# Kernel tuning notes

Hardware: AMD Instinct MI355X
Metric: run time of the kernel (lower is better)

The kernel has to match this reference:

```python
import jax, jax.numpy as jnp
import numpy as np

H = W = 256
WS = 8          # window size
SHIFT = 4       # shift size
HEADS = 8
DIM = 128
HD = DIM // HEADS
EPS = 1e-5


def _rel_index():
    # Swin-style relative position index, static constant (N=WS*WS)
    coords = np.stack(np.meshgrid(np.arange(WS), np.arange(WS), indexing='ij')).reshape(2, -1)
    rel = coords[:, :, None] - coords[:, None, :]        # (2, N, N)
    rel = rel + (WS - 1)
    return rel[0] * (2 * WS - 1) + rel[1]                # (N, N) in [0, (2WS-1)^2)

_REL_IDX = _rel_index()


def _ln(x, w, b):
    m = jnp.mean(x, axis=-1, keepdims=True)
    v = jnp.var(x, axis=-1, keepdims=True)
    return (x - m) * jax.lax.rsqrt(v + EPS) * w + b


def setup_inputs() -> dict:
    key = jax.random.key(0)
    ks = jax.random.split(key, 8)
    s = 0.02
    return {
        'x': jax.random.normal(ks[0], (2, H * W, DIM), jnp.float32),
        'norm1_w': jnp.ones((DIM,), jnp.float32),
        'norm1_b': jnp.zeros((DIM,), jnp.float32),
        'qkv_w': jax.random.normal(ks[1], (3 * DIM, DIM), jnp.float32) * s,
        'qkv_b': jnp.zeros((3 * DIM,), jnp.float32),
        'rel_bias_table': jax.random.normal(ks[2], ((2 * WS - 1) ** 2, HEADS), jnp.float32) * s,
        'proj_w': jax.random.normal(ks[3], (DIM, DIM), jnp.float32) * s,
        'proj_b': jnp.zeros((DIM,), jnp.float32),
        'norm2_w': jnp.ones((DIM,), jnp.float32),
        'norm2_b': jnp.zeros((DIM,), jnp.float32),
        'fc1_w': jax.random.normal(ks[4], (4 * DIM, DIM), jnp.float32) * s,
        'fc1_b': jnp.zeros((4 * DIM,), jnp.float32),
        'fc2_w': jax.random.normal(ks[5], (DIM, 4 * DIM), jnp.float32) * s,
        'fc2_b': jnp.zeros((DIM,), jnp.float32),
    }


def reference(x, norm1_w, norm1_b, qkv_w, qkv_b, rel_bias_table, proj_w, proj_b,
              norm2_w, norm2_b, fc1_w, fc1_b, fc2_w, fc2_b):
    B, L, C = x.shape
    N = WS * WS
    shortcut = x

    # norm1 -> spatial -> shift (roll only; original applies no attention mask)
    xs = _ln(x, norm1_w, norm1_b).reshape(B, H, W, C)
    xs = jnp.roll(xs, shift=(-SHIFT, -SHIFT), axis=(1, 2))

    # window partition: (B*nH*nW, N, C)
    win = xs.reshape(B, H // WS, WS, W // WS, WS, C)
    win = win.transpose(0, 1, 3, 2, 4, 5).reshape(-1, N, C)

    # window attention
    qkv = (win @ qkv_w.T + qkv_b).reshape(-1, N, 3, HEADS, HD)
    qkv = qkv.transpose(2, 0, 3, 1, 4)                   # (3, nWin, heads, N, hd)
    q, k, v = qkv[0], qkv[1], qkv[2]
    scale = HD ** -0.5
    attn = jnp.einsum('whnd,whmd->whnm', q * scale, k)   # (nWin, heads, N, N)
    bias = rel_bias_table[_REL_IDX]                      # (N, N, heads)
    attn = attn + bias.transpose(2, 0, 1)[None]
    attn = jax.nn.softmax(attn, axis=-1)
    out = jnp.einsum('whnm,whmd->whnd', attn, v)         # (nWin, heads, N, hd)
    out = out.transpose(0, 2, 1, 3).reshape(-1, N, C)
    out = out @ proj_w.T + proj_b

    # window reverse + un-shift
    out = out.reshape(B, H // WS, W // WS, WS, WS, C)
    out = out.transpose(0, 1, 3, 2, 4, 5).reshape(B, H, W, C)
    out = jnp.roll(out, shift=(SHIFT, SHIFT), axis=(1, 2)).reshape(B, L, C)

    x = shortcut + out

    # MLP (fc1 -> exact GELU -> fc2) with residual
    h = _ln(x, norm2_w, norm2_b)
    h = jax.nn.gelu(h @ fc1_w.T + fc1_b, approximate=False)
    h = h @ fc2_w.T + fc2_b
    return x + h
```

## Files before the change

### kernel.cpp

```cpp
#include <hip/hip_runtime.h>
#include <hip/hip_bf16.h>
#include <cmath>

#define LNEPS 1e-5f

typedef __attribute__((ext_vector_type(8))) short short8v;
typedef __attribute__((ext_vector_type(4))) float f32x4;

__device__ __forceinline__ unsigned short f2bf(float f){
  unsigned u = __float_as_uint(f);
  u += 0x7fffu + ((u >> 16) & 1u);
  return (unsigned short)(u >> 16);
}
__device__ __forceinline__ float gelu_f(float x){
  return 0.5f * x * (1.f + erff(x * 0.70710678118654752f));
}

__device__ __forceinline__ f32x4 mfma32(short8v a, short8v b, f32x4 c){
#ifdef __HIP_DEVICE_COMPILE__
  return __builtin_amdgcn_mfma_f32_16x16x32_bf16(a, b, c, 0, 0, 0);
#else
  return c;
#endif
}

__device__ __forceinline__ void stage128(const unsigned short* g, int ldg, short* lds){
#ifdef __HIP_DEVICE_COMPILE__
  const int t = threadIdx.x;
  const int wv = t >> 6;
  #pragma unroll
  for (int it = 0; it < 8; ++it) {
    const int flat = it * 256 + t;
    const int r = flat >> 4, c = flat & 15;
    const unsigned short* src = g + (size_t)r * ldg + ((c ^ (r & 7)) << 3);
    short* dst = lds + (size_t)(it * 256 + wv * 64) * 8;
    __builtin_amdgcn_global_load_lds(
        (const __attribute__((address_space(1))) void*)src,
        (__attribute__((address_space(3))) void*)dst, 16, 0, 0);
  }
#else
  (void)g; (void)ldg; (void)lds;
#endif
}
__device__ __forceinline__ void stage128_512(const unsigned short* g, int ldg, short* lds){
#ifdef __HIP_DEVICE_COMPILE__
  const int t = threadIdx.x;
  const int wv = t >> 6;
  #pragma unroll
  for (int it = 0; it < 4; ++it) {
    const int flat = it * 512 + t;
    const int r = flat >> 4, c = flat & 15;
    const unsigned short* src = g + (size_t)r * ldg + ((c ^ (r & 7)) << 3);
    short* dst = lds + (size_t)(it * 512 + wv * 64) * 8;
    __builtin_amdgcn_global_load_lds(
        (const __attribute__((address_space(1))) void*)src,
        (__attribute__((address_space(3))) void*)dst, 16, 0, 0);
  }
#else
  (void)g; (void)ldg; (void)lds;
#endif
}
__device__ __forceinline__ void stage64(const unsigned short* g, short* lds){
#ifdef __HIP_DEVICE_COMPILE__
  const int t = threadIdx.x;
  const int wv = t >> 6;
  #pragma unroll
  for (int it = 0; it < 4; ++it) {
    const int flat = it * 256 + t;
    const int r = flat >> 4, c = flat & 15;
    const unsigned short* src = g + (size_t)r * 128 + ((c ^ (r & 7)) << 3);
    short* dst = lds + (size_t)(it * 256 + wv * 64) * 8;
    __builtin_amdgcn_global_load_lds(
        (const __attribute__((address_space(1))) void*)src,
        (__attribute__((address_space(3))) void*)dst, 16, 0, 0);
  }
#else
  (void)g; (void)lds;
#endif
}
__device__ __forceinline__ short8v frag_ld(const short* lds, int row, int chunk){
  return *(const short8v*)((const char*)lds + row * 256 + ((chunk ^ (row & 7)) << 4));
}

__global__ __launch_bounds__(256) void k0_cvt(
    const float* __restrict__ qkvw, const float* __restrict__ pw,
    const float* __restrict__ w1, const float* __restrict__ w2,
    unsigned short* __restrict__ dst)
{
  const int i = (blockIdx.x * 256 + threadIdx.x) * 4;
  const float* src; int off;
  if (i < 49152)       { src = qkvw; off = i; }
  else if (i < 65536)  { src = pw;   off = i - 49152; }
  else if (i < 131072) { src = w1;   off = i - 65536; }
  else                 { src = w2;   off = i - 131072; }
  const float4 v = *(const float4*)(src + off);
  ushort4 o = { f2bf(v.x), f2bf(v.y), f2bf(v.z), f2bf(v.w) };
  *(ushort4*)(dst + i) = o;
}

__global__ __launch_bounds__(512, 2) void k23_qkv_attn(
    const float* __restrict__ x,
    const float* __restrict__ gw, const float* __restrict__ gb,
    const unsigned short* __restrict__ Wb,
    const float* __restrict__ bias,
    const float* __restrict__ table,
    unsigned short* __restrict__ attn)
{
  __shared__ __align__(16) short At[128 * 128];
  __shared__ __align__(16) short Bt[128 * 128];
  __shared__ __align__(16) short QKl[128 * 256];
  __shared__ float Tb[1800];
  const int t = threadIdx.x;
  const int row0 = blockIdx.x * 128;
  stage128_512(Wb, 128, At);
  for (int i = t; i < 1800; i += 512) Tb[i] = table[i];
  #pragma unroll
  for (int it = 0; it < 4; ++it) {
    const int flat = it * 512 + t;
    const int r = flat >> 4, c = flat & 15;
    const int row = row0 + r;
    const int wid = row >> 6, n = row & 63;
    const int b = wid >> 10, rem = wid & 1023;
    const int wh = rem >> 5, wwi = rem & 31;
    const int i2 = n >> 3, j2 = n & 7;
    const int sh = (wh * 8 + i2 + 4) & 255;
    const int sw = (wwi * 8 + j2 + 4) & 255;
    const float* src = x + (((size_t)b << 16) + sh * 256 + sw) * 128 + c * 8;
    const float4 a0 = *(const float4*)src;
    const float4 a1 = *(const float4*)(src + 4);
    float s  = a0.x + a0.y + a0.z + a0.w + a1.x + a1.y + a1.z + a1.w;
    float ss = a0.x*a0.x + a0.y*a0.y + a0.z*a0.z + a0.w*a0.w
             + a1.x*a1.x + a1.y*a1.y + a1.z*a1.z + a1.w*a1.w;
    s += __shfl_xor(s, 1); ss += __shfl_xor(ss, 1);
    s += __shfl_xor(s, 2); ss += __shfl_xor(ss, 2);
    s += __shfl_xor(s, 4); ss += __shfl_xor(ss, 4);
    s += __shfl_xor(s, 8); ss += __shfl_xor(ss, 8);
    const float mean = s * 0.0078125f;
    const float rstd = rsqrtf(ss * 0.0078125f - mean * mean + LNEPS);
    const float4 g0 = *(const float4*)(gw + c * 8), g1 = *(const float4*)(gw + c * 8 + 4);
    const float4 c0 = *(const float4*)(gb + c * 8), c1 = *(const float4*)(gb + c * 8 + 4);
    uint4 pk;
    pk.x = (unsigned)f2bf((a0.x - mean) * rstd * g0.x + c0.x)
         | ((unsigned)f2bf((a0.y - mean) * rstd * g0.y + c0.y) << 16);
    pk.y = (unsigned)f2bf((a0.z - mean) * rstd * g0.z + c0.z)
         | ((unsigned)f2bf((a0.w - mean) * rstd * g0.w + c0.w) << 16);
    pk.z = (unsigned)f2bf((a1.x - mean) * rstd * g1.x + c1.x)
         | ((unsigned)f2bf((a1.y - mean) * rstd * g1.y + c1.y) << 16);
    pk.w = (unsigned)f2bf((a1.z - mean) * rstd * g1.z + c1.z)
         | ((unsigned)f2bf((a1.w - mean) * rstd * g1.w + c1.w) << 16);
    *(uint4*)((char*)Bt + r * 256 + ((c ^ (r & 7)) << 4)) = pk;
  }
  __syncthreads();

  const int l = t & 63, w = t >> 6, w0 = w & 1, w1 = w >> 1;
  const int g = l >> 4, rl = l & 15;
  const f32x4 z = {0.f, 0.f, 0.f, 0.f};

  for (int nt = 0; nt < 3; ++nt) {
    f32x4 acc[4][2];
    #pragma unroll
    for (int i = 0; i < 4; ++i) { acc[i][0] = z; acc[i][1] = z; }
    #pragma unroll
    for (int kk = 0; kk < 4; ++kk) {
      short8v a[4], b[2];
      #pragma unroll
      for (int i = 0; i < 4; ++i) a[i] = frag_ld(At, w0 * 64 + i * 16 + rl, kk * 4 + g);
      #pragma unroll
      for (int j = 0; j < 2; ++j) b[j] = frag_ld(Bt, w1 * 32 + j * 16 + rl, kk * 4 + g);
      #pragma unroll
      for (int i = 0; i < 4; ++i)
        #pragma unroll
        for (int j = 0; j < 2; ++j)
          acc[i][j] = mfma32(a[i], b[j], acc[i][j]);
    }
    if (nt < 2) {
      #pragma unroll
      for (int i = 0; i < 4; ++i) {
        const int c = w0 * 64 + i * 16 + 4 * g;
        const float4 bv = *(const float4*)(bias + nt * 128 + c);
        const int chunk = nt * 16 + (c >> 3), inner = (c & 7) * 2;
        #pragma unroll
        for (int j = 0; j < 2; ++j) {
          const int r = w1 * 32 + j * 16 + rl;
          ushort4 o = { f2bf(acc[i][j][0] + bv.x), f2bf(acc[i][j][1] + bv.y),
                        f2bf(acc[i][j][2] + bv.z), f2bf(acc[i][j][3] + bv.w) };
          *(ushort4*)((char*)QKl + r * 512 + ((chunk ^ (r & 7)) << 4) + inner) = o;
        }
      }
      __syncthreads();
      stage128_512(Wb + (size_t)(nt + 1) * 16384, 128, At);
      __syncthreads();
    } else {
      __syncthreads();
      #pragma unroll
      for (int i = 0; i < 4; ++i) {
        const int c = w0 * 64 + i * 16 + 4 * g;
        const int h2 = c >> 4, db = c & 15;
        const float4 bv = *(const float4*)(bias + 256 + c);
        const float ba[4] = {bv.x, bv.y, bv.z, bv.w};
        #pragma unroll
        for (int j = 0; j < 2; ++j) {
          const int r = w1 * 32 + j * 16 + rl;
          const int wl = r >> 6, m = r & 63;
          char* vb = (char*)Bt + (wl * 8 + h2) * 2048;
          #pragma unroll
          for (int e = 0; e < 4; ++e) {
            const int d = db + e;
            *(unsigned short*)(vb + d * 128 + (((m >> 3) ^ (d & 7)) << 4) + (m & 7) * 2)
                = f2bf(acc[i][j][e] + ba[e]);
          }
        }
      }
      __syncthreads();
    }
  }

  const int h = w;
  char* Pw = (char*)At + w * 4096;
  const short8v zz = {0,0,0,0,0,0,0,0};
  for (int wl = 0; wl < 2; ++wl) {
    const int win = blockIdx.x * 2 + wl;
    short8v qf[4], kf[4];
    if (g < 2) {
      #pragma unroll
      for (int rf = 0; rf < 4; ++rf) {
        const int r = wl * 64 + rf * 16 + rl;
        qf[rf] = *(const short8v*)((char*)QKl + r * 512 + (((2 * h + g) ^ (r & 7)) << 4));
      }
      #pragma unroll
      for (int mf = 0; mf < 4; ++mf) {
        const int r = wl * 64 + mf * 16 + rl;
        kf[mf] = *(const short8v*)((char*)QKl + r * 512 + (((16 + 2 * h + g) ^ (r & 7)) << 4));
      }
    } else {
      #pragma unroll
      for (int i = 0; i < 4; ++i) { qf[i] = zz; kf[i] = zz; }
    }
    f32x4 s[4][4];
    #pragma unroll
    for (int mf = 0; mf < 4; ++mf)
      #pragma unroll
      for (int rf = 0; rf < 4; ++rf)
        s[mf][rf] = mfma32(kf[mf], qf[rf], z);
    float sum[4];
    #pragma unroll
    for (int rf = 0; rf < 4; ++rf) {
      const int r = rf * 16 + rl, i1 = r >> 3, j1 = r & 7;
      float mx = -1e30f;
      #pragma unroll
      for (int mf = 0; mf < 4; ++mf)
        #pragma unroll
        for (int e = 0; e < 4; ++e) {
          const int m = mf * 16 + g * 4 + e;
          const int i2 = m >> 3, j2 = m & 7;
          const float v = s[mf][rf][e] * 0.25f + Tb[((i1 - i2 + 7) * 15 + (j1 - j2 + 7)) * 8 + h];
          s[mf][rf][e] = v;
          mx = fmaxf(mx, v);
        }
      mx = fmaxf(mx, __shfl_xor(mx, 16));
      mx = fmaxf(mx, __shfl_xor(mx, 32));
      float sm = 0.f;
      #pragma unroll
      for (int mf = 0; mf < 4; ++mf)
        #pragma unroll
        for (int e = 0; e < 4; ++e) {
          const float ev = __expf(s[mf][rf][e] - mx);
          s[mf][rf][e] = ev;
          sm += ev;
        }
      sm += __shfl_xor(sm, 16);
      sm += __shfl_xor(sm, 32);
      sum[rf] = sm;
    }
    const char* vbase = (char*)Bt + (wl * 8 + h) * 2048;
    f32x4 o[4];
    #pragma unroll
    for (int rf = 0; rf < 4; ++rf) o[rf] = z;
    #pragma unroll
    for (int hm = 0; hm < 2; ++hm) {
      #pragma unroll
      for (int rf = 0; rf < 4; ++rf) {
        const int r = rf * 16 + rl;
        #pragma unroll
        for (int mfl = 0; mfl < 2; ++mfl) {
          const int mf = hm * 2 + mfl;
          uint2 u;
          u.x = (unsigned)f2bf(s[mf][rf][0]) | ((unsigned)f2bf(s[mf][rf][1]) << 16);
          u.y = (unsigned)f2bf(s[mf][rf][2]) | ((unsigned)f2bf(s[mf][rf][3]) << 16);
          *(uint2*)(Pw + r * 64 + (((mfl * 2 + (g >> 1)) ^ ((r >> 1) & 3)) << 4) + (g & 1) * 8) = u;
        }
      }
      const short8v va = *(const short8v*)(vbase + rl * 128 + (((hm * 4 + g) ^ (rl & 7)) << 4));
      #pragma unroll
      for (int rf = 0; rf < 4; ++rf) {
        const int r = rf * 16 + rl;
        const short8v pb = *(const short8v*)(Pw + r * 64 + ((g ^ ((r >> 1) & 3)) << 4));
        o[rf] = mfma32(va, pb, o[rf]);
      }
    }
    #pragma unroll
    for (int rf = 0; rf < 4; ++rf) {
      const float inv = 1.f / sum[rf];
      const int r = rf * 16 + rl;
      ushort4 ov = { f2bf(o[rf][0] * inv), f2bf(o[rf][1] * inv),
                     f2bf(o[rf][2] * inv), f2bf(o[rf][3] * inv) };
      *(ushort4*)(attn + ((size_t)win * 64 + r) * 128 + h * 16 + g * 4) = ov;
    }
  }
}

__global__ __launch_bounds__(256, 2) void k45_proj_mlp(
    const unsigned short* __restrict__ A,
    const unsigned short* __restrict__ pwb,
    const float* __restrict__ pb,
    const float* __restrict__ xin,
    const float* __restrict__ gw, const float* __restrict__ gb,
    const unsigned short* __restrict__ w1b, const float* __restrict__ b1,
    const unsigned short* __restrict__ w2b, const float* __restrict__ b2,
    float* __restrict__ out)
{
  __shared__ __align__(16) short Xt[64 * 128];
  __shared__ __align__(16) short Ht[64 * 128];
  __shared__ __align__(16) short Wt[128 * 128];
  __shared__ float2 Gt[1024];
  __shared__ float2 Red[64 * 8];
  const int t = threadIdx.x;
  const int row0 = blockIdx.x * 64;
  stage128(pwb, 128, Wt);
  stage64(A + (size_t)row0 * 128, Ht);
  #pragma unroll
  for (int i = t; i < 1024; i += 256) {
    const float x0 = (float)i * 0.0078125f - 4.f;
    const float g0 = gelu_f(x0);
    Gt[i] = make_float2(g0, gelu_f(x0 + 0.0078125f) - g0);
  }
  const int l = t & 63, w = t >> 6, w0 = w & 1, w1 = w >> 1;
  const int g = l >> 4, rl = l & 15;
  size_t obase[2];
  float4 xv[4][2];
  #pragma unroll
  for (int j = 0; j < 2; ++j) {
    const int r = row0 + w1 * 32 + j * 16 + rl;
    const int wn = r >> 6, n = r & 63;
    const int b_ = wn >> 10, rem = wn & 1023;
    const int wh = rem >> 5, ww = rem & 31;
    const int si = n >> 3, sj = n & 7;
    const int hd = (wh * 8 + si + 4) & 255;
    const int wd = (ww * 8 + sj + 4) & 255;
    obase[j] = (((size_t)b_ << 16) + hd * 256 + wd) * 128;
    #pragma unroll
    for (int i = 0; i < 4; ++i)
      xv[i][j] = *(const float4*)(xin + obase[j] + w0 * 64 + i * 16 + 4 * g);
  }
  __syncthreads();
  const f32x4 z = {0.f, 0.f, 0.f, 0.f};
  f32x4 x2r[4][2];
  #pragma unroll
  for (int i = 0; i < 4; ++i) { x2r[i][0] = z; x2r[i][1] = z; }
  #pragma unroll
  for (int kk = 0; kk < 4; ++kk) {
    short8v a[4], b[2];
    #pragma unroll
    for (int i = 0; i < 4; ++i) a[i] = frag_ld(Wt, w0 * 64 + i * 16 + rl, kk * 4 + g);
    #pragma unroll
    for (int j = 0; j < 2; ++j) b[j] = frag_ld(Ht, w1 * 32 + j * 16 + rl, kk * 4 + g);
    #pragma unroll
    for (int i = 0; i < 4; ++i)
      #pragma unroll
      for (int j = 0; j < 2; ++j)
        x2r[i][j] = mfma32(a[i], b[j], x2r[i][j]);
  }
  #pragma unroll
  for (int i = 0; i < 4; ++i) {
    const float4 bv = *(const float4*)(pb + w0 * 64 + i * 16 + 4 * g);
    #pragma unroll
    for (int j = 0; j < 2; ++j) {
      x2r[i][j][0] += xv[i][j].x + bv.x;
      x2r[i][j][1] += xv[i][j].y + bv.y;
      x2r[i][j][2] += xv[i][j].z + bv.z;
      x2r[i][j][3] += xv[i][j].w + bv.w;
    }
  }
  #pragma unroll
  for (int j = 0; j < 2; ++j) {
    float s = 0.f, ss = 0.f;
    #pragma unroll
    for (int i = 0; i < 4; ++i)
      #pragma unroll
      for (int e = 0; e < 4; ++e) { const float v = x2r[i][j][e]; s += v; ss += v * v; }
    Red[(w1 * 32 + j * 16 + rl) * 8 + (w0 * 4 + g)] = make_float2(s, ss);
  }
  __syncthreads();
  float mean[2], rstd[2];
  #pragma unroll
  for (int j = 0; j < 2; ++j) {
    const float2* rp = &Red[(w1 * 32 + j * 16 + rl) * 8];
    float s = 0.f, ss = 0.f;
    #pragma unroll
    for (int k = 0; k < 8; ++k) { s += rp[k].x; ss += rp[k].y; }
    mean[j] = s * 0.0078125f;
    rstd[j] = rsqrtf(ss * 0.0078125f - mean[j] * mean[j] + LNEPS);
  }
  #pragma unroll
  for (int i = 0; i < 4; ++i) {
    const int c = w0 * 64 + i * 16 + 4 * g;
    const float4 g4 = *(const float4*)(gw + c);
    const float4 c4 = *(const float4*)(gb + c);
    #pragma unroll
    for (int j = 0; j < 2; ++j) {
      const int r = w1 * 32 + j * 16 + rl;
      ushort4 p;
      p.x = f2bf((x2r[i][j][0] - mean[j]) * rstd[j] * g4.x + c4.x);
      p.y = f2bf((x2r[i][j][1] - mean[j]) * rstd[j] * g4.y + c4.y);
      p.z = f2bf((x2r[i][j][2] - mean[j]) * rstd[j] * g4.z + c4.z);
      p.w = f2bf((x2r[i][j][3] - mean[j]) * rstd[j] * g4.w + c4.w);
      const int chunk = c >> 3, inner = (c & 7) * 2;
      *(ushort4*)((char*)Xt + r * 256 + ((chunk ^ (r & 7)) << 4) + inner) = p;
    }
  }
  f32x4 oacc[4][2];
  #pragma unroll
  for (int i = 0; i < 4; ++i) { oacc[i][0] = z; oacc[i][1] = z; }
  for (int sb = 0; sb < 4; ++sb) {
    __syncthreads();
    stage128(w1b + (size_t)sb * 128 * 128, 128, Wt);
    __syncthreads();
    f32x4 hacc[4][2];
    #pragma unroll
    for (int i = 0; i < 4; ++i) { hacc[i][0] = z; hacc[i][1] = z; }
    #pragma unroll
    for (int kk = 0; kk < 4; ++kk) {
      short8v a[4], b[2];
      #pragma unroll
      for (int i = 0; i < 4; ++i) a[i] = frag_ld(Wt, w0 * 64 + i * 16 + rl, kk * 4 + g);
      #pragma unroll
      for (int j = 0; j < 2; ++j) b[j] = frag_ld(Xt, w1 * 32 + j * 16 + rl, kk * 4 + g);
      #pragma unroll
      for (int i = 0; i < 4; ++i)
        #pragma unroll
        for (int j = 0; j < 2; ++j)
          hacc[i][j] = mfma32(a[i], b[j], hacc[i][j]);
    }
    __syncthreads();
    #pragma unroll
    for (int i = 0; i < 4; ++i) {
      const int cl = w0 * 64 + i * 16 + 4 * g;
      const float4 b1v = *(const float4*)(b1 + sb * 128 + cl);
      const float ba[4] = {b1v.x, b1v.y, b1v.z, b1v.w};
      #pragma unroll
      for (int j = 0; j < 2; ++j) {
        const int r = w1 * 32 + j * 16 + rl;
        unsigned short pe[4];
        #pragma unroll
        for (int e = 0; e < 4; ++e) {
          const float xh = hacc[i][j][e] + ba[e];
          float tq = fmaf(xh, 128.f, 512.f);
          tq = fminf(fmaxf(tq, 0.f), 1023.99f);
          const float fi = floorf(tq);
          const float2 ent = Gt[(int)fi];
          float gv = fmaf(tq - fi, ent.y, ent.x);
          gv = xh > 3.98f ? xh : gv;
          pe[e] = f2bf(gv);
        }
        ushort4 p = { pe[0], pe[1], pe[2], pe[3] };
        const int chunk = cl >> 3, inner = (cl & 7) * 2;
        *(ushort4*)((char*)Ht + r * 256 + ((chunk ^ (r & 7)) << 4) + inner) = p;
      }
    }
    stage128(w2b + (size_t)sb * 128, 512, Wt);
    __syncthreads();
    #pragma unroll
    for (int kk = 0; kk < 4; ++kk) {
      short8v a[4], b[2];
      #pragma unroll
      for (int i = 0; i < 4; ++i) a[i] = frag_ld(Wt, w0 * 64 + i * 16 + rl, kk * 4 + g);
      #pragma unroll
      for (int j = 0; j < 2; ++j) b[j] = frag_ld(Ht, w1 * 32 + j * 16 + rl, kk * 4 + g);
      #pragma unroll
      for (int i = 0; i < 4; ++i)
        #pragma unroll
        for (int j = 0; j < 2; ++j)
          oacc[i][j] = mfma32(a[i], b[j], oacc[i][j]);
    }
  }
  #pragma unroll
  for (int i = 0; i < 4; ++i) {
    const int c = w0 * 64 + i * 16 + 4 * g;
    const float4 bv = *(const float4*)(b2 + c);
    #pragma unroll
    for (int j = 0; j < 2; ++j) {
      float4 o = { x2r[i][j][0] + oacc[i][j][0] + bv.x,
                   x2r[i][j][1] + oacc[i][j][1] + bv.y,
                   x2r[i][j][2] + oacc[i][j][2] + bv.z,
                   x2r[i][j][3] + oacc[i][j][3] + bv.w };
      *(float4*)(out + obase[j] + c) = o;
    }
  }
}

extern "C" void kernel_launch(void* const* d_in, const int* in_sizes, int n_in,
                              void* d_out, int out_size, void* d_ws, size_t ws_size,
                              hipStream_t stream)
{
  const float* x    = (const float*)d_in[0];
  const float* n1w  = (const float*)d_in[1];
  const float* n1b  = (const float*)d_in[2];
  const float* qkvw = (const float*)d_in[3];
  const float* qkvB = (const float*)d_in[4];
  const float* relb = (const float*)d_in[5];
  const float* pw   = (const float*)d_in[6];
  const float* pb   = (const float*)d_in[7];
  const float* n2w  = (const float*)d_in[8];
  const float* n2b  = (const float*)d_in[9];
  const float* w1   = (const float*)d_in[10];
  const float* b1   = (const float*)d_in[11];
  const float* w2   = (const float*)d_in[12];
  const float* b2   = (const float*)d_in[13];
  float* out = (float*)d_out;

  unsigned short* winb = (unsigned short*)d_ws;
  unsigned short* wb   = winb + 16777216;
  unsigned short* qkvw_b = wb;
  unsigned short* pw_b   = wb + 49152;
  unsigned short* w1_b   = wb + 65536;
  unsigned short* w2_b   = wb + 131072;

  k0_cvt<<<192, 256, 0, stream>>>(qkvw, pw, w1, w2, wb);
  k23_qkv_attn<<<1024, 512, 0, stream>>>(x, n1w, n1b, qkvw_b, qkvB, relb, winb);
  k45_proj_mlp<<<2048, 256, 0, stream>>>(winb, pw_b, pb, x, n2w, n2b,
                                         w1_b, b1, w2_b, b2, out);
}
```

Before: 177.2 us.

## Fuse window attention with projection and MLP into one kernel

Merges the QKV+attention kernel and the proj+MLP kernel into a single 512-thread kernel, so attention outputs stay in LDS instead of round-tripping a 32MB bf16 buffer through global memory. The MLP stage is re-tiled so each wave owns 16 rows across all 128 output columns, which lets LayerNorm2 reduce with wave shuffles instead of an LDS reduction. The costs are a roughly 143KB LDS footprint that permits only one block per CU despite the launch bound of 2, a larger live register set, and a longer serial dependency chain per block.

```diff
diff --git a/kernel.cpp b/kernel.cpp
--- a/kernel.cpp
+++ b/kernel.cpp
@@ -24,24 +24,6 @@
 #endif
 }
 
-__device__ __forceinline__ void stage128(const unsigned short* g, int ldg, short* lds){
-#ifdef __HIP_DEVICE_COMPILE__
-  const int t = threadIdx.x;
-  const int wv = t >> 6;
-  #pragma unroll
-  for (int it = 0; it < 8; ++it) {
-    const int flat = it * 256 + t;
-    const int r = flat >> 4, c = flat & 15;
-    const unsigned short* src = g + (size_t)r * ldg + ((c ^ (r & 7)) << 3);
-    short* dst = lds + (size_t)(it * 256 + wv * 64) * 8;
-    __builtin_amdgcn_global_load_lds(
-        (const __attribute__((address_space(1))) void*)src,
-        (__attribute__((address_space(3))) void*)dst, 16, 0, 0);
-  }
-#else
-  (void)g; (void)ldg; (void)lds;
-#endif
-}
 __device__ __forceinline__ void stage128_512(const unsigned short* g, int ldg, short* lds){
 #ifdef __HIP_DEVICE_COMPILE__
   const int t = threadIdx.x;
@@ -58,24 +40,6 @@
   }
 #else
   (void)g; (void)ldg; (void)lds;
-#endif
-}
-__device__ __forceinline__ void stage64(const unsigned short* g, short* lds){
-#ifdef __HIP_DEVICE_COMPILE__
-  const int t = threadIdx.x;
-  const int wv = t >> 6;
-  #pragma unroll
-  for (int it = 0; it < 4; ++it) {
-    const int flat = it * 256 + t;
-    const int r = flat >> 4, c = flat & 15;
-    const unsigned short* src = g + (size_t)r * 128 + ((c ^ (r & 7)) << 3);
-    short* dst = lds + (size_t)(it * 256 + wv * 64) * 8;
-    __builtin_amdgcn_global_load_lds(
-        (const __attribute__((address_space(1))) void*)src,
-        (__attribute__((address_space(3))) void*)dst, 16, 0, 0);
-  }
-#else
-  (void)g; (void)lds;
 #endif
 }
 __device__ __forceinline__ short8v frag_ld(const short* lds, int row, int chunk){
@@ -98,22 +62,32 @@
   *(ushort4*)(dst + i) = o;
 }
 
-__global__ __launch_bounds__(512, 2) void k23_qkv_attn(
+__global__ __launch_bounds__(512, 2) void kfull(
     const float* __restrict__ x,
-    const float* __restrict__ gw, const float* __restrict__ gb,
-    const unsigned short* __restrict__ Wb,
-    const float* __restrict__ bias,
+    const float* __restrict__ g1w, const float* __restrict__ g1b,
+    const unsigned short* __restrict__ qkvWb, const float* __restrict__ qkvB,
     const float* __restrict__ table,
-    unsigned short* __restrict__ attn)
+    const unsigned short* __restrict__ pwb, const float* __restrict__ pb,
+    const float* __restrict__ g2w, const float* __restrict__ g2b,
+    const unsigned short* __restrict__ w1b, const float* __restrict__ b1,
+    const unsigned short* __restrict__ w2b, const float* __restrict__ b2,
+    float* __restrict__ out)
 {
-  __shared__ __align__(16) short At[128 * 128];
-  __shared__ __align__(16) short Bt[128 * 128];
-  __shared__ __align__(16) short QKl[128 * 256];
-  __shared__ float Tb[1800];
+  __shared__ __align__(16) char LP[146464];
+  short*  At  = (short*)LP;
+  short*  Bt  = (short*)(LP + 32768);
+  short*  QKl = (short*)(LP + 65536);
+  float*  Tb  = (float*)(LP + 131072);
+  float2* Gt  = (float2*)(LP + 138272);
   const int t = threadIdx.x;
   const int row0 = blockIdx.x * 128;
-  stage128_512(Wb, 128, At);
+  stage128_512(qkvWb, 128, At);
   for (int i = t; i < 1800; i += 512) Tb[i] = table[i];
+  for (int i = t; i < 1024; i += 512) {
+    const float x0 = (float)i * 0.0078125f - 4.f;
+    const float g0 = gelu_f(x0);
+    Gt[i] = make_float2(g0, gelu_f(x0 + 0.0078125f) - g0);
+  }
   #pragma unroll
   for (int it = 0; it < 4; ++it) {
     const int flat = it * 512 + t;
@@ -137,8 +111,8 @@
     s += __shfl_xor(s, 8); ss += __shfl_xor(ss, 8);
     const float mean = s * 0.0078125f;
     const float rstd = rsqrtf(ss * 0.0078125f - mean * mean + LNEPS);
-    const float4 g0 = *(const float4*)(gw + c * 8), g1 = *(const float4*)(gw + c * 8 + 4);
-    const float4 c0 = *(const float4*)(gb + c * 8), c1 = *(const float4*)(gb + c * 8 + 4);
+    const float4 g0 = *(const float4*)(g1w + c * 8), g1 = *(const float4*)(g1w + c * 8 + 4);
+    const float4 c0 = *(const float4*)(g1b + c * 8), c1 = *(const float4*)(g1b + c * 8 + 4);
     uint4 pk;
     pk.x = (unsigned)f2bf((a0.x - mean) * rstd * g0.x + c0.x)
          | ((unsigned)f2bf((a0.y - mean) * rstd * g0.y + c0.y) << 16);
@@ -152,7 +126,7 @@
   }
   __syncthreads();
 
-  const int l = t & 63, w = t >> 6, w0 = w & 1, w1 = w >> 1;
+  const int l = t & 63, w = t >> 6, w0 = w & 1, w1q = w >> 1;
   const int g = l >> 4, rl = l & 15;
   const f32x4 z = {0.f, 0.f, 0.f, 0.f};
 
@@ -166,7 +140,7 @@
       #pragma unroll
       for (int i = 0; i < 4; ++i) a[i] = frag_ld(At, w0 * 64 + i * 16 + rl, kk * 4 + g);
       #pragma unroll
-      for (int j = 0; j < 2; ++j) b[j] = frag_ld(Bt, w1 * 32 + j * 16 + rl, kk * 4 + g);
+      for (int j = 0; j < 2; ++j) b[j] = frag_ld(Bt, w1q * 32 + j * 16 + rl, kk * 4 + g);
       #pragma unroll
       for (int i = 0; i < 4; ++i)
         #pragma unroll
@@ -177,18 +151,18 @@
       #pragma unroll
       for (int i = 0; i < 4; ++i) {
         const int c = w0 * 64 + i * 16 + 4 * g;
-        const float4 bv = *(const float4*)(bias + nt * 128 + c);
+        const float4 bv = *(const float4*)(qkvB + nt * 128 + c);
         const int chunk = nt * 16 + (c >> 3), inner = (c & 7) * 2;
         #pragma unroll
         for (int j = 0; j < 2; ++j) {
-          const int r = w1 * 32 + j * 16 + rl;
+          const int r = w1q * 32 + j * 16 + rl;
           ushort4 o = { f2bf(acc[i][j][0] + bv.x), f2bf(acc[i][j][1] + bv.y),
                         f2bf(acc[i][j][2] + bv.z), f2bf(acc[i][j][3] + bv.w) };
           *(ushort4*)((char*)QKl + r * 512 + ((chunk ^ (r & 7)) << 4) + inner) = o;
         }
       }
       __syncthreads();
-      stage128_512(Wb + (size_t)(nt + 1) * 16384, 128, At);
+      stage128_512(qkvWb + (size_t)(nt + 1) * 16384, 128, At);
       __syncthreads();
     } else {
       __syncthreads();
@@ -196,11 +170,11 @@
       for (int i = 0; i < 4; ++i) {
         const int c = w0 * 64 + i * 16 + 4 * g;
         const int h2 = c >> 4, db = c & 15;
-        const float4 bv = *(const float4*)(bias + 256 + c);
+        const float4 bv = *(const float4*)(qkvB + 256 + c);
         const float ba[4] = {bv.x, bv.y, bv.z, bv.w};
         #pragma unroll
         for (int j = 0; j < 2; ++j) {
-          const int r = w1 * 32 + j * 16 + rl;
+          const int r = w1q * 32 + j * 16 + rl;
           const int wl = r >> 6, m = r & 63;
           char* vb = (char*)Bt + (wl * 8 + h2) * 2048;
           #pragma unroll
@@ -218,8 +192,8 @@
   const int h = w;
   char* Pw = (char*)At + w * 4096;
   const short8v zz = {0,0,0,0,0,0,0,0};
+  f32x4 o2[2][4];
   for (int wl = 0; wl < 2; ++wl) {
-    const int win = blockIdx.x * 2 + wl;
     short8v qf[4], kf[4];
     if (g < 2) {
       #pragma unroll
@@ -294,207 +268,138 @@
       #pragma unroll
       for (int rf = 0; rf < 4; ++rf) {
         const int r = rf * 16 + rl;
-        const short8v pb = *(const short8v*)(Pw + r * 64 + ((g ^ ((r >> 1) & 3)) << 4));
-        o[rf] = mfma32(va, pb, o[rf]);
+        const short8v pbv = *(const short8v*)(Pw + r * 64 + ((g ^ ((r >> 1) & 3)) << 4));
+        o[rf] = mfma32(va, pbv, o[rf]);
       }
     }
     #pragma unroll
     for (int rf = 0; rf < 4; ++rf) {
       const float inv = 1.f / sum[rf];
-      const int r = rf * 16 + rl;
-      ushort4 ov = { f2bf(o[rf][0] * inv), f2bf(o[rf][1] * inv),
-                     f2bf(o[rf][2] * inv), f2bf(o[rf][3] * inv) };
-      *(ushort4*)(attn + ((size_t)win * 64 + r) * 128 + h * 16 + g * 4) = ov;
-    }
-  }
-}
-
-__global__ __launch_bounds__(256, 2) void k45_proj_mlp(
-    const unsigned short* __restrict__ A,
-    const unsigned short* __restrict__ pwb,
-    const float* __restrict__ pb,
-    const float* __restrict__ xin,
-    const float* __restrict__ gw, const float* __restrict__ gb,
-    const unsigned short* __restrict__ w1b, const float* __restrict__ b1,
-    const unsigned short* __restrict__ w2b, const float* __restrict__ b2,
-    float* __restrict__ out)
-{
-  __shared__ __align__(16) short Xt[64 * 128];
-  __shared__ __align__(16) short Ht[64 * 128];
-  __shared__ __align__(16) short Wt[128 * 128];
-  __shared__ float2 Gt[1024];
-  __shared__ float2 Red[64 * 8];
-  const int t = threadIdx.x;
-  const int row0 = blockIdx.x * 64;
-  stage128(pwb, 128, Wt);
-  stage64(A + (size_t)row0 * 128, Ht);
-  #pragma unroll
-  for (int i = t; i < 1024; i += 256) {
-    const float x0 = (float)i * 0.0078125f - 4.f;
-    const float g0 = gelu_f(x0);
-    Gt[i] = make_float2(g0, gelu_f(x0 + 0.0078125f) - g0);
-  }
-  const int l = t & 63, w = t >> 6, w0 = w & 1, w1 = w >> 1;
-  const int g = l >> 4, rl = l & 15;
-  size_t obase[2];
-  float4 xv[4][2];
-  #pragma unroll
-  for (int j = 0; j < 2; ++j) {
-    const int r = row0 + w1 * 32 + j * 16 + rl;
+      o2[wl][rf][0] = o[rf][0] * inv; o2[wl][rf][1] = o[rf][1] * inv;
+      o2[wl][rf][2] = o[rf][2] * inv; o2[wl][rf][3] = o[rf][3] * inv;
+    }
+  }
+  __syncthreads();
+  stage128_512(pwb, 128, At);
+  #pragma unroll
+  for (int wl = 0; wl < 2; ++wl)
+    #pragma unroll
+    for (int rf = 0; rf < 4; ++rf) {
+      const int r = wl * 64 + rf * 16 + rl;
+      const int c = h * 16 + 4 * g;
+      const int chunk = c >> 3, inner = (c & 7) * 2;
+      ushort4 ov = { f2bf(o2[wl][rf][0]), f2bf(o2[wl][rf][1]),
+                     f2bf(o2[wl][rf][2]), f2bf(o2[wl][rf][3]) };
+      *(ushort4*)((char*)QKl + r * 256 + ((chunk ^ (r & 7)) << 4) + inner) = ov;
+    }
+  __syncthreads();
+
+  const int wrow = w * 16 + rl;
+  size_t obase;
+  {
+    const int r = row0 + wrow;
     const int wn = r >> 6, n = r & 63;
     const int b_ = wn >> 10, rem = wn & 1023;
     const int wh = rem >> 5, ww = rem & 31;
     const int si = n >> 3, sj = n & 7;
     const int hd = (wh * 8 + si + 4) & 255;
     const int wd = (ww * 8 + sj + 4) & 255;
-    obase[j] = (((size_t)b_ << 16) + hd * 256 + wd) * 128;
-    #pragma unroll
-    for (int i = 0; i < 4; ++i)
-      xv[i][j] = *(const float4*)(xin + obase[j] + w0 * 64 + i * 16 + 4 * g);
-  }
-  __syncthreads();
-  const f32x4 z = {0.f, 0.f, 0.f, 0.f};
-  f32x4 x2r[4][2];
-  #pragma unroll
-  for (int i = 0; i < 4; ++i) { x2r[i][0] = z; x2r[i][1] = z; }
+    obase = (((size_t)b_ << 16) + hd * 256 + wd) * 128;
+  }
+  f32x4 x2r[8];
+  #pragma unroll
+  for (int i = 0; i < 8; ++i) x2r[i] = z;
   #pragma unroll
   for (int kk = 0; kk < 4; ++kk) {
-    short8v a[4], b[2];
-    #pragma unroll
-    for (int i = 0; i < 4; ++i) a[i] = frag_ld(Wt, w0 * 64 + i * 16 + rl, kk * 4 + g);
-    #pragma unroll
-    for (int j = 0; j < 2; ++j) b[j] = frag_ld(Ht, w1 * 32 + j * 16 + rl, kk * 4 + g);
-    #pragma unroll
-    for (int i = 0; i < 4; ++i)
-      #pragma unroll
-      for (int j = 0; j < 2; ++j)
-        x2r[i][j] = mfma32(a[i], b[j], x2r[i][j]);
-  }
-  #pragma unroll
-  for (int i = 0; i < 4; ++i) {
-    const float4 bv = *(const float4*)(pb + w0 * 64 + i * 16 + 4 * g);
-    #pragma unroll
-    for (int j = 0; j < 2; ++j) {
-      x2r[i][j][0] += xv[i][j].x + bv.x;
-      x2r[i][j][1] += xv[i][j].y + bv.y;
-      x2r[i][j][2] += xv[i][j].z + bv.z;
-      x2r[i][j][3] += xv[i][j].w + bv.w;
-    }
-  }
-  #pragma unroll
-  for (int j = 0; j < 2; ++j) {
-    float s = 0.f, ss = 0.f;
-    #pragma unroll
-    for (int i = 0; i < 4; ++i)
-      #pragma unroll
-      for (int e = 0; e < 4; ++e) { const float v = x2r[i][j][e]; s += v; ss += v * v; }
-    Red[(w1 * 32 + j * 16 + rl) * 8 + (w0 * 4 + g)] = make_float2(s, ss);
-  }
-  __syncthreads();
-  float mean[2], rstd[2];
-  #pragma unroll
-  for (int j = 0; j < 2; ++j) {
-    const float2* rp = &Red[(w1 * 32 + j * 16 + rl) * 8];
-    float s = 0.f, ss = 0.f;
-    #pragma unroll
-    for (int k = 0; k < 8; ++k) { s += rp[k].x; ss += rp[k].y; }
-    mean[j] = s * 0.0078125f;
-    rstd[j] = rsqrtf(ss * 0.0078125f - mean[j] * mean[j] + LNEPS);
-  }
-  #pragma unroll
-  for (int i = 0; i < 4; ++i) {
-    const int c = w0 * 64 + i * 16 + 4 * g;
-    const float4 g4 = *(const float4*)(gw + c);
-    const float4 c4 = *(const float4*)(gb + c);
-    #pragma unroll
-    for (int j = 0; j < 2; ++j) {
-      const int r = w1 * 32 + j * 16 + rl;
-      ushort4 p;
-      p.x = f2bf((x2r[i][j][0] - mean[j]) * rstd[j] * g4.x + c4.x);
-      p.y = f2bf((x2r[i][j][1] - mean[j]) * rstd[j] * g4.y + c4.y);
-      p.z = f2bf((x2r[i][j][2] - mean[j]) * rstd[j] * g4.z + c4.z);
-      p.w = f2bf((x2r[i][j][3] - mean[j]) * rstd[j] * g4.w + c4.w);
-      const int chunk = c >> 3, inner = (c & 7) * 2;
-      *(ushort4*)((char*)Xt + r * 256 + ((chunk ^ (r & 7)) << 4) + inner) = p;
-    }
-  }
-  f32x4 oacc[4][2];
-  #pragma unroll
-  for (int i = 0; i < 4; ++i) { oacc[i][0] = z; oacc[i][1] = z; }
+    const short8v b = frag_ld(QKl, wrow, kk * 4 + g);
+    #pragma unroll
+    for (int i = 0; i < 8; ++i)
+      x2r[i] = mfma32(frag_ld(At, i * 16 + rl, kk * 4 + g), b, x2r[i]);
+  }
+  float s2 = 0.f, ss2 = 0.f;
+  #pragma unroll
+  for (int i = 0; i < 8; ++i) {
+    const int c = i * 16 + 4 * g;
+    const float4 xv = *(const float4*)(x + obase + c);
+    const float4 bv = *(const float4*)(pb + c);
+    x2r[i][0] += xv.x + bv.x; x2r[i][1] += xv.y + bv.y;
+    x2r[i][2] += xv.z + bv.z; x2r[i][3] += xv.w + bv.w;
+    #pragma unroll
+    for (int e = 0; e < 4; ++e) { const float v = x2r[i][e]; s2 += v; ss2 += v * v; }
+  }
+  s2 += __shfl_xor(s2, 16); ss2 += __shfl_xor(ss2, 16);
+  s2 += __shfl_xor(s2, 32); ss2 += __shfl_xor(ss2, 32);
+  const float mean2 = s2 * 0.0078125f;
+  const float rstd2 = rsqrtf(ss2 * 0.0078125f - mean2 * mean2 + LNEPS);
+  #pragma unroll
+  for (int i = 0; i < 8; ++i) {
+    const int c = i * 16 + 4 * g;
+    const float4 g4 = *(const float4*)(g2w + c);
+    const float4 c4 = *(const float4*)(g2b + c);
+    ushort4 p;
+    p.x = f2bf((x2r[i][0] - mean2) * rstd2 * g4.x + c4.x);
+    p.y = f2bf((x2r[i][1] - mean2) * rstd2 * g4.y + c4.y);
+    p.z = f2bf((x2r[i][2] - mean2) * rstd2 * g4.z + c4.z);
+    p.w = f2bf((x2r[i][3] - mean2) * rstd2 * g4.w + c4.w);
+    const int chunk = c >> 3, inner = (c & 7) * 2;
+    *(ushort4*)((char*)Bt + wrow * 256 + ((chunk ^ (wrow & 7)) << 4) + inner) = p;
+  }
+  f32x4 oacc[8];
+  #pragma unroll
+  for (int i = 0; i < 8; ++i) oacc[i] = z;
   for (int sb = 0; sb < 4; ++sb) {
     __syncthreads();
-    stage128(w1b + (size_t)sb * 128 * 128, 128, Wt);
+    stage128_512(w1b + (size_t)sb * 16384, 128, At);
     __syncthreads();
-    f32x4 hacc[4][2];
-    #pragma unroll
-    for (int i = 0; i < 4; ++i) { hacc[i][0] = z; hacc[i][1] = z; }
+    f32x4 hacc[8];
+    #pragma unroll
+    for (int i = 0; i < 8; ++i) hacc[i] = z;
     #pragma unroll
     for (int kk = 0; kk < 4; ++kk) {
-      short8v a[4], b[2];
-      #pragma unroll
-      for (int i = 0; i < 4; ++i) a[i] = frag_ld(Wt, w0 * 64 + i * 16 + rl, kk * 4 + g);
-      #pragma unroll
-      for (int j = 0; j < 2; ++j) b[j] = frag_ld(Xt, w1 * 32 + j * 16 + rl, kk * 4 + g);
-      #pragma unroll
-      for (int i = 0; i < 4; ++i)
-        #pragma unroll
-        for (int j = 0; j < 2; ++j)
-          hacc[i][j] = mfma32(a[i], b[j], hacc[i][j]);
+      const short8v b = frag_ld(Bt, wrow, kk * 4 + g);
+      #pragma unroll
+      for (int i = 0; i < 8; ++i)
+        hacc[i] = mfma32(frag_ld(At, i * 16 + rl, kk * 4 + g), b, hacc[i]);
     }
     __syncthreads();
-    #pragma unroll
-    for (int i = 0; i < 4; ++i) {
-      const int cl = w0 * 64 + i * 16 + 4 * g;
-      const float4 b1v = *(const float4*)(b1 + sb * 128 + cl);
+    stage128_512(w2b + (size_t)sb * 128, 512, At);
+    #pragma unroll
+    for (int i = 0; i < 8; ++i) {
+      const int c = i * 16 + 4 * g;
+      const float4 b1v = *(const float4*)(b1 + sb * 128 + c);
       const float ba[4] = {b1v.x, b1v.y, b1v.z, b1v.w};
-      #pragma unroll
-      for (int j = 0; j < 2; ++j) {
-        const int r = w1 * 32 + j * 16 + rl;
-        unsigned short pe[4];
-        #pragma unroll
-        for (int e = 0; e < 4; ++e) {
-          const float xh = hacc[i][j][e] + ba[e];
-          float tq = fmaf(xh, 128.f, 512.f);
-          tq = fminf(fmaxf(tq, 0.f), 1023.99f);
-          const float fi = floorf(tq);
-          const float2 ent = Gt[(int)fi];
-          float gv = fmaf(tq - fi, ent.y, ent.x);
-          gv = xh > 3.98f ? xh : gv;
-          pe[e] = f2bf(gv);
-        }
-        ushort4 p = { pe[0], pe[1], pe[2], pe[3] };
-        const int chunk = cl >> 3, inner = (cl & 7) * 2;
-        *(ushort4*)((char*)Ht + r * 256 + ((chunk ^ (r & 7)) << 4) + inner) = p;
-      }
-    }
-    stage128(w2b + (size_t)sb * 128, 512, Wt);
+      unsigned short pe[4];
+      #pragma unroll
+      for (int e = 0; e < 4; ++e) {
+        const float xh = hacc[i][e] + ba[e];
+        float tq = fmaf(xh, 128.f, 512.f);
+        tq = fminf(fmaxf(tq, 0.f), 1023.99f);
+        const float fi = floorf(tq);
+        const float2 ent = Gt[(int)fi];
+        float gv = fmaf(tq - fi, ent.y, ent.x);
+        gv = xh > 3.98f ? xh : gv;
+        pe[e] = f2bf(gv);
+      }
+      ushort4 p = { pe[0], pe[1], pe[2], pe[3] };
+      const int chunk = c >> 3, inner = (c & 7) * 2;
+      *(ushort4*)((char*)QKl + wrow * 256 + ((chunk ^ (wrow & 7)) << 4) + inner) = p;
+    }
     __syncthreads();
     #pragma unroll
     for (int kk = 0; kk < 4; ++kk) {
-      short8v a[4], b[2];
-      #pragma unroll
-      for (int i = 0; i < 4; ++i) a[i] = frag_ld(Wt, w0 * 64 + i * 16 + rl, kk * 4 + g);
-      #pragma unroll
-      for (int j = 0; j < 2; ++j) b[j] = frag_ld(Ht, w1 * 32 + j * 16 + rl, kk * 4 + g);
-      #pragma unroll
-      for (int i = 0; i < 4; ++i)
-        #pragma unroll
-        for (int j = 0; j < 2; ++j)
-          oacc[i][j] = mfma32(a[i], b[j], oacc[i][j]);
-    }
-  }
-  #pragma unroll
-  for (int i = 0; i < 4; ++i) {
-    const int c = w0 * 64 + i * 16 + 4 * g;
+      const short8v b = frag_ld(QKl, wrow, kk * 4 + g);
+      #pragma unroll
+      for (int i = 0; i < 8; ++i)
+        oacc[i] = mfma32(frag_ld(At, i * 16 + rl, kk * 4 + g), b, oacc[i]);
+    }
+  }
+  #pragma unroll
+  for (int i = 0; i < 8; ++i) {
+    const int c = i * 16 + 4 * g;
     const float4 bv = *(const float4*)(b2 + c);
-    #pragma unroll
-    for (int j = 0; j < 2; ++j) {
-      float4 o = { x2r[i][j][0] + oacc[i][j][0] + bv.x,
-                   x2r[i][j][1] + oacc[i][j][1] + bv.y,
-                   x2r[i][j][2] + oacc[i][j][2] + bv.z,
-                   x2r[i][j][3] + oacc[i][j][3] + bv.w };
-      *(float4*)(out + obase[j] + c) = o;
-    }
+    float4 o = { x2r[i][0] + oacc[i][0] + bv.x, x2r[i][1] + oacc[i][1] + bv.y,
+                 x2r[i][2] + oacc[i][2] + bv.z, x2r[i][3] + oacc[i][3] + bv.w };
+    *(float4*)(out + obase + c) = o;
   }
 }
 
@@ -518,15 +423,13 @@
   const float* b2   = (const float*)d_in[13];
   float* out = (float*)d_out;
 
-  unsigned short* winb = (unsigned short*)d_ws;
-  unsigned short* wb   = winb + 16777216;
+  unsigned short* wb = (unsigned short*)d_ws;
   unsigned short* qkvw_b = wb;
   unsigned short* pw_b   = wb + 49152;
   unsigned short* w1_b   = wb + 65536;
   unsigned short* w2_b   = wb + 131072;
 
   k0_cvt<<<192, 256, 0, stream>>>(qkvw, pw, w1, w2, wb);
-  k23_qkv_attn<<<1024, 512, 0, stream>>>(x, n1w, n1b, qkvw_b, qkvB, relb, winb);
-  k45_proj_mlp<<<2048, 256, 0, stream>>>(winb, pw_b, pb, x, n2w, n2b,
-                                         w1_b, b1, w2_b, b2, out);
-}
+  kfull<<<1024, 512, 0, stream>>>(x, n1w, n1b, qkvw_b, qkvB, relb,
+                                  pw_b, pb, n2w, n2b, w1_b, b1, w2_b, b2, out);
+}
```

After: 195.9 us. 1.11x slower.
